# Kernel tuning notes

Measured on AMD Instinct MI355X. Metric: run time of the kernel, lower is better.

## Reference

```python
import jax, jax.numpy as jnp
import numpy as np

K, Q, DIM = 64, 128, 1024
TF_W, DE_W, FFT_W = 1.0, 0.8, 0.6  # opt.TF_weight / DE_weight / FFT_weight


def setup_inputs() -> dict:
    key = jax.random.key(0)
    ks = jax.random.split(key, 9)
    def feats(k):
        return jax.random.normal(k, (K, Q, DIM), dtype=jnp.float32)
    def protos(k):
        return jax.random.normal(k, (K, DIM), dtype=jnp.float32)
    def var(k):
        # positive variances, bounded away from zero
        return jax.random.uniform(k, (K,), dtype=jnp.float32) + 0.5
    return {
        "TFq_output": feats(ks[0]), "TFs_proto": protos(ks[1]), "TF_variance": var(ks[2]),
        "DEq_output": feats(ks[3]), "DEs_proto": protos(ks[4]), "DE_variance": var(ks[5]),
        "FFTq_output": feats(ks[6]), "FFTs_proto": protos(ks[7]), "FFT_variance": var(ks[8]),
    }


def _mah_dist(xq, proto, variance):
    # ||x - p||^2 / var via expansion: avoids materializing (num, protonum, dim)
    x2 = jnp.sum(xq * xq, axis=1, keepdims=True)            # (num, 1)
    p2 = jnp.sum(proto * proto, axis=1)[None, :]            # (1, protonum)
    xp = xq @ proto.T                                       # (num, protonum)
    return (x2 - 2.0 * xp + p2) / variance[None, :]


def _modality(xq, proto, variance, w):
    logits = -_mah_dist(xq, proto, variance)
    pred = w * jax.nn.softmax(logits, axis=1)
    mahloss = -(w * jax.nn.log_softmax(logits, axis=1))
    return pred, mahloss


def reference(TFq_output, TFs_proto, TF_variance,
              DEq_output, DEs_proto, DE_variance,
              FFTq_output, FFTs_proto, FFT_variance):
    k, q, _ = TFq_output.shape
    y = jnp.repeat(jnp.arange(k), q)                         # (k*q,)

    tf_pred, tf_loss = _modality(TFq_output.reshape(k * q, -1), TFs_proto, TF_variance, TF_W)
    de_pred, de_loss = _modality(DEq_output.reshape(k * q, -1), DEs_proto, DE_variance, DE_W)
    fft_pred, fft_loss = _modality(FFTq_output.reshape(k * q, -1), FFTs_proto, FFT_variance, FFT_W)

    fusion_loss = tf_loss + de_loss + fft_loss               # (k*q, k)
    loss = jnp.take_along_axis(fusion_loss, y[:, None], axis=1).squeeze(-1).mean()

    pred_mah = tf_pred + de_pred + fft_pred
    pred = jnp.argmax(pred_mah, axis=1)
    acc = (pred == y).astype(jnp.float32).mean()
    return (loss, acc)
```

## Files before the change

kernel.cpp:

```cpp
#include <hip/hip_runtime.h>


typedef _Float16 half8 __attribute__((ext_vector_type(8)));
typedef float    floatx4 __attribute__((ext_vector_type(4)));

#define NCLS   64
#define QPC    128
#define DIM    1024
#define NROWS  (NCLS * QPC)
#define NRT    (NROWS / 16)
#define CHUNK  256
#define NCHUNK (DIM / CHUNK)
#define NKC    (CHUNK / 32)
#define UW     264

#define OFF_W    0
#define W_BYTES  (3 * NCLS * DIM * 2)
#define OFF_P2   W_BYTES
#define OFF_PRED 397312
#define PRED_BYTES (3 * NROWS * NCLS * 4)
#define OFF_LOSS (OFF_PRED + PRED_BYTES)
#define OFF_CNT  (OFF_LOSS + 1536 * 4)
#define WS_NEED  (OFF_CNT + 64 * 4)

__device__ __forceinline__ void dma16(const float* g, float* l) {
    __builtin_amdgcn_global_load_lds(
        (const __attribute__((address_space(1))) void*)g,
        (__attribute__((address_space(3))) void*)l,
        16, 0, 0);
}

__global__ __launch_bounds__(64) void prep_protos(
    const float* __restrict__ Ptf, const float* __restrict__ Pde,
    const float* __restrict__ Pff, _Float16* __restrict__ W,
    float* __restrict__ p2)
{
    const int m    = blockIdx.x >> 5;
    const int kcg  = blockIdx.x & 31;
    const int lane = threadIdx.x;
    const int l15  = lane & 15;
    const int quad = lane >> 4;
    const float* __restrict__ P = (m == 0) ? Ptf : (m == 1) ? Pde : Pff;

    #pragma unroll
    for (int t = 0; t < 4; ++t) {
        const float* src = P + (size_t)(t * 16 + l15) * DIM + kcg * 32 + quad * 8;
        const float4 b0 = *reinterpret_cast<const float4*>(src);
        const float4 b1 = *reinterpret_cast<const float4*>(src + 4);
        half8 h;
        h[0] = (_Float16)b0.x; h[1] = (_Float16)b0.y;
        h[2] = (_Float16)b0.z; h[3] = (_Float16)b0.w;
        h[4] = (_Float16)b1.x; h[5] = (_Float16)b1.y;
        h[6] = (_Float16)b1.z; h[7] = (_Float16)b1.w;
        *reinterpret_cast<half8*>(W + ((size_t)(m * 32 + kcg) * 4 + t) * 512 + lane * 8) = h;

        float s = b0.x*b0.x + b0.y*b0.y + b0.z*b0.z + b0.w*b0.w
                + b1.x*b1.x + b1.y*b1.y + b1.z*b1.z + b1.w*b1.w;
        s += __shfl_xor(s, 16);
        s += __shfl_xor(s, 32);
        if (quad == 0) atomicAdd(&p2[m * 64 + t * 16 + l15], s);
    }
}

__global__ __launch_bounds__(128) void fusion_main(
    const float* __restrict__ Xtf, const float* __restrict__ Vtf,
    const float* __restrict__ Xde, const float* __restrict__ Vde,
    const float* __restrict__ Xff, const float* __restrict__ Vff,
    const _Float16* __restrict__ W, const float* __restrict__ p2g,
    float* __restrict__ predOut,
    float* __restrict__ lossPart)
{
    __shared__ float chunkBuf[16 * UW];
    __shared__ float mxW[2][16], sW[2][16];
    __shared__ float lossW[2];

    const int tid  = threadIdx.x;
    const int w    = tid >> 6;
    const int lane = tid & 63;
    const int l15  = lane & 15;
    const int quad = lane >> 4;
    const int m    = blockIdx.x >> 9;
    const int rt   = blockIdx.x & 511;
    const int rowBase = rt * 16;

    const float* __restrict__ X = (m == 0) ? Xtf : (m == 1) ? Xde : Xff;
    const float* __restrict__ V = (m == 0) ? Vtf : (m == 1) ? Vde : Vff;
    const float  wgt = (m == 0) ? 1.0f : (m == 1) ? 0.8f : 0.6f;

    floatx4 d[2];
    d[0] = (floatx4){0.f, 0.f, 0.f, 0.f};
    d[1] = (floatx4){0.f, 0.f, 0.f, 0.f};
    float x2p = 0.0f;

    #pragma unroll 1
    for (int c = 0; c < NCHUNK; ++c) {
        __syncthreads();
        const float* gbase = X + (size_t)rowBase * DIM + c * CHUNK + lane * 4;
        #pragma unroll
        for (int r8 = 0; r8 < 8; ++r8) {
            const int r = w * 8 + r8;
            dma16(gbase + (size_t)r * DIM, &chunkBuf[r * UW]);
        }
        __syncthreads();

        #pragma unroll
        for (int kc = 0; kc < NKC; ++kc) {
            const int off = l15 * UW + kc * 32 + quad * 8;
            const float4 a0 = *reinterpret_cast<const float4*>(&chunkBuf[off]);
            const float4 a1 = *reinterpret_cast<const float4*>(&chunkBuf[off + 4]);

            const int kcg = c * NKC + kc;
            half8 bf[2];
            #pragma unroll
            for (int t = 0; t < 2; ++t)
                bf[t] = *reinterpret_cast<const half8*>(
                    W + ((size_t)(m * 32 + kcg) * 4 + (w * 2 + t)) * 512 + lane * 8);

            x2p += a0.x*a0.x + a0.y*a0.y + a0.z*a0.z + a0.w*a0.w
                 + a1.x*a1.x + a1.y*a1.y + a1.z*a1.z + a1.w*a1.w;

            half8 af;
            af[0] = (_Float16)a0.x; af[1] = (_Float16)a0.y;
            af[2] = (_Float16)a0.z; af[3] = (_Float16)a0.w;
            af[4] = (_Float16)a1.x; af[5] = (_Float16)a1.y;
            af[6] = (_Float16)a1.z; af[7] = (_Float16)a1.w;

            d[0] = __builtin_amdgcn_mfma_f32_16x16x32_f16(af, bf[0], d[0], 0, 0, 0);
            d[1] = __builtin_amdgcn_mfma_f32_16x16x32_f16(af, bf[1], d[1], 0, 0, 0);
        }
    }

    x2p += __shfl_xor(x2p, 16);
    x2p += __shfl_xor(x2p, 32);
    float x2r[4];
    #pragma unroll
    for (int r = 0; r < 4; ++r) x2r[r] = __shfl(x2p, quad * 4 + r);

    float vc[2], p2c[2];
    #pragma unroll
    for (int t = 0; t < 2; ++t) {
        const int col = w * 32 + t * 16 + l15;
        vc[t]  = V[col];
        p2c[t] = p2g[m * 64 + col];
    }

    float lg[4][2];
    #pragma unroll
    for (int r = 0; r < 4; ++r)
        #pragma unroll
        for (int t = 0; t < 2; ++t)
            lg[r][t] = (2.0f * d[t][r] - x2r[r] - p2c[t]) / vc[t];

    #pragma unroll
    for (int r = 0; r < 4; ++r) {
        float mx = fmaxf(lg[r][0], lg[r][1]);
        #pragma unroll
        for (int dl = 1; dl <= 8; dl <<= 1) mx = fmaxf(mx, __shfl_xor(mx, dl));
        if (l15 == 0) mxW[w][quad * 4 + r] = mx;
    }
    __syncthreads();
    float gmx[4];
    #pragma unroll
    for (int r = 0; r < 4; ++r) {
        const int row = quad * 4 + r;
        gmx[r] = fmaxf(mxW[0][row], mxW[1][row]);
        float s = expf(lg[r][0] - gmx[r]) + expf(lg[r][1] - gmx[r]);
        #pragma unroll
        for (int dl = 1; dl <= 8; dl <<= 1) s += __shfl_xor(s, dl);
        if (l15 == 0) sW[w][row] = s;
    }
    __syncthreads();

    const int y = rowBase >> 7;
    float lossAcc = 0.0f;
    #pragma unroll
    for (int r = 0; r < 4; ++r) {
        const int row = quad * 4 + r;
        const float lse = gmx[r] + logf(sW[0][row] + sW[1][row]);
        if (w == (y >> 5) && l15 == (y & 15))
            lossAcc += wgt * (lse - lg[r][(y >> 4) & 1]);
        const int R = rowBase + row;
        #pragma unroll
        for (int t = 0; t < 2; ++t)
            predOut[((size_t)m * NROWS + R) * 64 + w * 32 + t * 16 + l15] =
                wgt * expf(lg[r][t] - lse);
    }

    #pragma unroll
    for (int dl = 1; dl <= 32; dl <<= 1) lossAcc += __shfl_xor(lossAcc, dl);
    if (lane == 0) lossW[w] = lossAcc;
    __syncthreads();
    if (tid == 0) lossPart[blockIdx.x] = lossW[0] + lossW[1];
}

__global__ __launch_bounds__(256) void finalize1(
    const float* __restrict__ pred, float* __restrict__ cntPart)
{
    const int tid  = threadIdx.x;
    const int w    = tid >> 6;
    const int lane = tid & 63;
    float cnt = 0.0f;
    #pragma unroll 1
    for (int i = 0; i < 32; ++i) {
        const int R = blockIdx.x * 128 + w * 32 + i;
        float p = pred[(size_t)R * 64 + lane]
                + pred[((size_t)NROWS + R) * 64 + lane]
                + pred[((size_t)2 * NROWS + R) * 64 + lane];
        float bv = p; int bc = lane;
        #pragma unroll
        for (int dl = 1; dl <= 32; dl <<= 1) {
            const float ov = __shfl_xor(bv, dl);
            const int   oc = __shfl_xor(bc, dl);
            if (ov > bv || (ov == bv && oc < bc)) { bv = ov; bc = oc; }
        }
        if (lane == 0 && bc == (R >> 7)) cnt += 1.0f;
    }
    #pragma unroll
    for (int dl = 1; dl <= 32; dl <<= 1) cnt += __shfl_xor(cnt, dl);
    __shared__ float sc[4];
    if (lane == 0) sc[w] = cnt;
    __syncthreads();
    if (tid == 0) cntPart[blockIdx.x] = sc[0] + sc[1] + sc[2] + sc[3];
}

__global__ __launch_bounds__(256) void finalize2(
    const float* __restrict__ lossPart, const float* __restrict__ cntPart,
    float* __restrict__ out)
{
    const int tid  = threadIdx.x;
    const int lane = tid & 63;
    const int w    = tid >> 6;
    float l = 0.0f, c = 0.0f;
    for (int i = tid; i < 1536; i += 256) l += lossPart[i];
    if (tid < 64) c = cntPart[tid];
    #pragma unroll
    for (int dl = 1; dl <= 32; dl <<= 1) {
        l += __shfl_xor(l, dl);
        c += __shfl_xor(c, dl);
    }
    __shared__ float sl[4], sc[4];
    if (lane == 0) { sl[w] = l; sc[w] = c; }
    __syncthreads();
    if (tid == 0) {
        out[0] = (sl[0] + sl[1] + sl[2] + sl[3]) * (1.0f / NROWS);
        out[1] = (sc[0] + sc[1] + sc[2] + sc[3]) * (1.0f / NROWS);
    }
}

#define NWAVES 12
#define KSPLIT 4
#define KSLICE (DIM / KSPLIT)
#define NITER  (KSLICE / 32)
#define DSTRIDE 17
#define PSTRIDE 65

__global__ __launch_bounds__(NWAVES * 64) void fusion_loss_fallback(
    const float* __restrict__ Xtf, const float* __restrict__ Ptf, const float* __restrict__ Vtf,
    const float* __restrict__ Xde, const float* __restrict__ Pde, const float* __restrict__ Vde,
    const float* __restrict__ Xff, const float* __restrict__ Pff, const float* __restrict__ Vff,
    float* __restrict__ out)
{
    __shared__ float dpart[NWAVES][64 * DSTRIDE];
    __shared__ float x2part[NWAVES][16];
    __shared__ float p2part[NWAVES][64];
    __shared__ float predL[16 * PSTRIDE];
    __shared__ float lossL;

    const int tid  = threadIdx.x;
    const int wave = tid >> 6;
    const int lane = tid & 63;
    const int l15  = lane & 15;
    const int quad = lane >> 4;
    const int m    = wave >> 2;
    const int kq   = wave & 3;
    const int rowBase = blockIdx.x * 16;

    for (int i = tid; i < 16 * PSTRIDE; i += NWAVES * 64) predL[i] = 0.0f;
    if (tid == 0) lossL = 0.0f;

    const float* __restrict__ X = (m == 0) ? Xtf : (m == 1) ? Xde : Xff;
    const float* __restrict__ P = (m == 0) ? Ptf : (m == 1) ? Pde : Pff;
    const float* __restrict__ V = (m == 0) ? Vtf : (m == 1) ? Vde : Vff;
    const float  w = (m == 0) ? 1.0f : (m == 1) ? 0.8f : 0.6f;

    floatx4 d[4];
    #pragma unroll
    for (int t = 0; t < 4; ++t) d[t] = (floatx4){0.f, 0.f, 0.f, 0.f};
    float x2p    = 0.0f;
    float p2p[4] = {0.f, 0.f, 0.f, 0.f};

    const float* xrow = X + (size_t)(rowBase + l15) * DIM + kq * KSLICE + quad * 8;
    const float* prow[4];
    #pragma unroll
    for (int t = 0; t < 4; ++t)
        prow[t] = P + (size_t)(t * 16 + l15) * DIM + kq * KSLICE + quad * 8;

    #pragma unroll 2
    for (int kc = 0; kc < NITER; ++kc) {
        const int ko = kc * 32;
        const float4 a0 = *reinterpret_cast<const float4*>(xrow + ko);
        const float4 a1 = *reinterpret_cast<const float4*>(xrow + ko + 4);
        float4 b0[4], b1[4];
        #pragma unroll
        for (int t = 0; t < 4; ++t) {
            b0[t] = *reinterpret_cast<const float4*>(prow[t] + ko);
            b1[t] = *reinterpret_cast<const float4*>(prow[t] + ko + 4);
        }
        x2p += a0.x*a0.x + a0.y*a0.y + a0.z*a0.z + a0.w*a0.w
             + a1.x*a1.x + a1.y*a1.y + a1.z*a1.z + a1.w*a1.w;
        half8 af;
        af[0] = (_Float16)a0.x; af[1] = (_Float16)a0.y;
        af[2] = (_Float16)a0.z; af[3] = (_Float16)a0.w;
        af[4] = (_Float16)a1.x; af[5] = (_Float16)a1.y;
        af[6] = (_Float16)a1.z; af[7] = (_Float16)a1.w;
        #pragma unroll
        for (int t = 0; t < 4; ++t) {
            p2p[t] += b0[t].x*b0[t].x + b0[t].y*b0[t].y + b0[t].z*b0[t].z + b0[t].w*b0[t].w
                    + b1[t].x*b1[t].x + b1[t].y*b1[t].y + b1[t].z*b1[t].z + b1[t].w*b1[t].w;
            half8 bf;
            bf[0] = (_Float16)b0[t].x; bf[1] = (_Float16)b0[t].y;
            bf[2] = (_Float16)b0[t].z; bf[3] = (_Float16)b0[t].w;
            bf[4] = (_Float16)b1[t].x; bf[5] = (_Float16)b1[t].y;
            bf[6] = (_Float16)b1[t].z; bf[7] = (_Float16)b1[t].w;
            d[t] = __builtin_amdgcn_mfma_f32_16x16x32_f16(af, bf, d[t], 0, 0, 0);
        }
    }

    x2p += __shfl_xor(x2p, 16);
    x2p += __shfl_xor(x2p, 32);
    #pragma unroll
    for (int t = 0; t < 4; ++t) {
        p2p[t] += __shfl_xor(p2p[t], 16);
        p2p[t] += __shfl_xor(p2p[t], 32);
    }
    {
        float* dp = &dpart[wave][lane * DSTRIDE];
        #pragma unroll
        for (int t = 0; t < 4; ++t)
            *reinterpret_cast<float4*>(dp + t * 4) =
                make_float4(d[t][0], d[t][1], d[t][2], d[t][3]);
        if (quad == 0) {
            x2part[wave][l15] = x2p;
            #pragma unroll
            for (int t = 0; t < 4; ++t) p2part[wave][t * 16 + l15] = p2p[t];
        }
    }
    __syncthreads();

    const int y = rowBase >> 7;

    if (kq == 0) {
        floatx4 dsum[4];
        #pragma unroll
        for (int t = 0; t < 4; ++t) dsum[t] = (floatx4){0.f, 0.f, 0.f, 0.f};
        float x2r[4] = {0.f, 0.f, 0.f, 0.f};
        float p2c[4] = {0.f, 0.f, 0.f, 0.f};
        #pragma unroll
        for (int k2 = 0; k2 < KSPLIT; ++k2) {
            const int wv = m * 4 + k2;
            const float* src = &dpart[wv][lane * DSTRIDE];
            #pragma unroll
            for (int t = 0; t < 4; ++t) {
                const float4 v = *reinterpret_cast<const float4*>(src + t * 4);
                dsum[t][0] += v.x; dsum[t][1] += v.y; dsum[t][2] += v.z; dsum[t][3] += v.w;
            }
            #pragma unroll
            for (int r = 0; r < 4; ++r) x2r[r] += x2part[wv][quad * 4 + r];
            #pragma unroll
            for (int t = 0; t < 4; ++t) p2c[t] += p2part[wv][t * 16 + l15];
        }
        float vc[4];
        #pragma unroll
        for (int t = 0; t < 4; ++t) vc[t] = V[t * 16 + l15];

        float lossAcc = 0.0f;
        #pragma unroll
        for (int r = 0; r < 4; ++r) {
            float lg[4];
            #pragma unroll
            for (int t = 0; t < 4; ++t)
                lg[t] = (2.0f * dsum[t][r] - x2r[r] - p2c[t]) / vc[t];
            float mx = fmaxf(fmaxf(lg[0], lg[1]), fmaxf(lg[2], lg[3]));
            #pragma unroll
            for (int dl = 1; dl <= 8; dl <<= 1) mx = fmaxf(mx, __shfl_xor(mx, dl));
            float s = expf(lg[0] - mx) + expf(lg[1] - mx)
                    + expf(lg[2] - mx) + expf(lg[3] - mx);
            #pragma unroll
            for (int dl = 1; dl <= 8; dl <<= 1) s += __shfl_xor(s, dl);
            const float lse = mx + logf(s);
            const int row = quad * 4 + r;
            #pragma unroll
            for (int t = 0; t < 4; ++t) {
                const int col = t * 16 + l15;
                if (col == y) lossAcc += w * (lse - lg[t]);
                atomicAdd(&predL[row * PSTRIDE + col], w * expf(lg[t] - lse));
            }
        }
        #pragma unroll
        for (int dl = 1; dl <= 32; dl <<= 1) lossAcc += __shfl_xor(lossAcc, dl);
        if (lane == 0) atomicAdd(&lossL, lossAcc);
    }
    __syncthreads();

    if (wave == 0) {
        float cnt = 0.0f;
        #pragma unroll 1
        for (int r = 0; r < 16; ++r) {
            float bv = predL[r * PSTRIDE + lane];
            int   bc = lane;
            #pragma unroll
            for (int dl = 1; dl <= 32; dl <<= 1) {
                const float ov = __shfl_xor(bv, dl);
                const int   oc = __shfl_xor(bc, dl);
                if (ov > bv || (ov == bv && oc < bc)) { bv = ov; bc = oc; }
            }
            if (lane == 0 && bc == y) cnt += 1.0f;
        }
        if (lane == 0) {
            atomicAdd(&out[0], lossL * (1.0f / NROWS));
            atomicAdd(&out[1], cnt * (1.0f / NROWS));
        }
    }
}

extern "C" void kernel_launch(void* const* d_in, const int* in_sizes, int n_in,
                              void* d_out, int out_size, void* d_ws, size_t ws_size,
                              hipStream_t stream) {
    const float* Xtf = (const float*)d_in[0];
    const float* Ptf = (const float*)d_in[1];
    const float* Vtf = (const float*)d_in[2];
    const float* Xde = (const float*)d_in[3];
    const float* Pde = (const float*)d_in[4];
    const float* Vde = (const float*)d_in[5];
    const float* Xff = (const float*)d_in[6];
    const float* Pff = (const float*)d_in[7];
    const float* Vff = (const float*)d_in[8];
    float* out = (float*)d_out;

    if (ws_size >= (size_t)WS_NEED) {
        char* ws = (char*)d_ws;
        _Float16* W    = (_Float16*)(ws + OFF_W);
        float*    p2   = (float*)(ws + OFF_P2);
        float*    pred = (float*)(ws + OFF_PRED);
        float*    lossP= (float*)(ws + OFF_LOSS);
        float*    cntP = (float*)(ws + OFF_CNT);

        hipMemsetAsync(p2, 0, 3 * NCLS * sizeof(float), stream);
        prep_protos<<<dim3(96), dim3(64), 0, stream>>>(Ptf, Pde, Pff, W, p2);
        fusion_main<<<dim3(3 * NRT), dim3(128), 0, stream>>>(
            Xtf, Vtf, Xde, Vde, Xff, Vff, W, p2, pred, lossP);
        finalize1<<<dim3(NROWS / 128), dim3(256), 0, stream>>>(pred, cntP);
        finalize2<<<dim3(1), dim3(256), 0, stream>>>(lossP, cntP, out);
    } else {
        hipMemsetAsync(out, 0, 2 * sizeof(float), stream);
        fusion_loss_fallback<<<dim3(NROWS / 16), dim3(NWAVES * 64), 0, stream>>>(
            Xtf, Ptf, Vtf, Xde, Pde, Vde, Xff, Pff, Vff, out);
    }
}
```

Measured before the change: 175.5 us.

## Split GEMM over K into two blocks and move softmax/loss into finalize

```diff
diff --git a/kernel.cpp b/kernel.cpp
--- a/kernel.cpp
+++ b/kernel.cpp
@@ -9,19 +9,18 @@
 #define DIM    1024
 #define NROWS  (NCLS * QPC)
 #define NRT    (NROWS / 16)
-#define CHUNK  256
-#define NCHUNK (DIM / CHUNK)
-#define NKC    (CHUNK / 32)
-#define UW     264
-
-#define OFF_W    0
-#define W_BYTES  (3 * NCLS * DIM * 2)
-#define OFF_P2   W_BYTES
-#define OFF_PRED 397312
-#define PRED_BYTES (3 * NROWS * NCLS * 4)
-#define OFF_LOSS (OFF_PRED + PRED_BYTES)
-#define OFF_CNT  (OFF_LOSS + 1536 * 4)
-#define WS_NEED  (OFF_CNT + 64 * 4)
+#define UW     260
+
+#define OFF_W     0
+#define W_BYTES   (3 * NCLS * DIM * 2)
+#define OFF_P2    W_BYTES
+#define OFF_PD    397312
+#define PD_BYTES  (3 * NRT * 2 * 16 * 64 * 4)
+#define OFF_PX2   (OFF_PD + PD_BYTES)
+#define PX2_BYTES (3 * NRT * 2 * 16 * 4)
+#define OFF_LP    (OFF_PX2 + PX2_BYTES)
+#define OFF_CP    (OFF_LP + NRT * 4)
+#define WS_NEED   (OFF_CP + NRT * 4)
 
 __device__ __forceinline__ void dma16(const float* g, float* l) {
     __builtin_amdgcn_global_load_lds(
@@ -62,59 +61,46 @@
     }
 }
 
-__global__ __launch_bounds__(128) void fusion_main(
-    const float* __restrict__ Xtf, const float* __restrict__ Vtf,
-    const float* __restrict__ Xde, const float* __restrict__ Vde,
-    const float* __restrict__ Xff, const float* __restrict__ Vff,
-    const _Float16* __restrict__ W, const float* __restrict__ p2g,
-    float* __restrict__ predOut,
-    float* __restrict__ lossPart)
+__global__ __launch_bounds__(256) void fusion_main(
+    const float* __restrict__ Xtf, const float* __restrict__ Xde,
+    const float* __restrict__ Xff, const _Float16* __restrict__ W,
+    float* __restrict__ pd, float* __restrict__ px2)
 {
     __shared__ float chunkBuf[16 * UW];
-    __shared__ float mxW[2][16], sW[2][16];
-    __shared__ float lossW[2];
 
     const int tid  = threadIdx.x;
     const int w    = tid >> 6;
     const int lane = tid & 63;
     const int l15  = lane & 15;
     const int quad = lane >> 4;
-    const int m    = blockIdx.x >> 9;
-    const int rt   = blockIdx.x & 511;
+    const int b    = blockIdx.x;
+    const int m    = b >> 10;
+    const int rt   = (b & 1023) >> 1;
+    const int ks   = b & 1;
     const int rowBase = rt * 16;
 
     const float* __restrict__ X = (m == 0) ? Xtf : (m == 1) ? Xde : Xff;
-    const float* __restrict__ V = (m == 0) ? Vtf : (m == 1) ? Vde : Vff;
-    const float  wgt = (m == 0) ? 1.0f : (m == 1) ? 0.8f : 0.6f;
-
-    floatx4 d[2];
-    d[0] = (floatx4){0.f, 0.f, 0.f, 0.f};
-    d[1] = (floatx4){0.f, 0.f, 0.f, 0.f};
+
+    floatx4 d = (floatx4){0.f, 0.f, 0.f, 0.f};
     float x2p = 0.0f;
 
     #pragma unroll 1
-    for (int c = 0; c < NCHUNK; ++c) {
+    for (int c = 0; c < 2; ++c) {
+        if (c) __syncthreads();
+        const float* gb = X + (size_t)(rowBase + w * 4) * DIM + ks * 512 + c * 256 + lane * 4;
+        #pragma unroll
+        for (int r4 = 0; r4 < 4; ++r4)
+            dma16(gb + (size_t)r4 * DIM, &chunkBuf[(w * 4 + r4) * UW]);
         __syncthreads();
-        const float* gbase = X + (size_t)rowBase * DIM + c * CHUNK + lane * 4;
-        #pragma unroll
-        for (int r8 = 0; r8 < 8; ++r8) {
-            const int r = w * 8 + r8;
-            dma16(gbase + (size_t)r * DIM, &chunkBuf[r * UW]);
-        }
-        __syncthreads();
-
-        #pragma unroll
-        for (int kc = 0; kc < NKC; ++kc) {
+
+        const int kbase = m * 32 + ks * 16 + c * 8;
+        #pragma unroll
+        for (int kc = 0; kc < 8; ++kc) {
             const int off = l15 * UW + kc * 32 + quad * 8;
             const float4 a0 = *reinterpret_cast<const float4*>(&chunkBuf[off]);
             const float4 a1 = *reinterpret_cast<const float4*>(&chunkBuf[off + 4]);
-
-            const int kcg = c * NKC + kc;
-            half8 bf[2];
-            #pragma unroll
-            for (int t = 0; t < 2; ++t)
-                bf[t] = *reinterpret_cast<const half8*>(
-                    W + ((size_t)(m * 32 + kcg) * 4 + (w * 2 + t)) * 512 + lane * 8);
+            const half8 bf = *reinterpret_cast<const half8*>(
+                W + ((size_t)(kbase + kc) * 4 + w) * 512 + lane * 8);
 
             x2p += a0.x*a0.x + a0.y*a0.y + a0.z*a0.z + a0.w*a0.w
                  + a1.x*a1.x + a1.y*a1.y + a1.z*a1.z + a1.w*a1.w;
@@ -125,102 +111,84 @@
             af[4] = (_Float16)a1.x; af[5] = (_Float16)a1.y;
             af[6] = (_Float16)a1.z; af[7] = (_Float16)a1.w;
 
-            d[0] = __builtin_amdgcn_mfma_f32_16x16x32_f16(af, bf[0], d[0], 0, 0, 0);
-            d[1] = __builtin_amdgcn_mfma_f32_16x16x32_f16(af, bf[1], d[1], 0, 0, 0);
+            d = __builtin_amdgcn_mfma_f32_16x16x32_f16(af, bf, d, 0, 0, 0);
         }
     }
 
     x2p += __shfl_xor(x2p, 16);
     x2p += __shfl_xor(x2p, 32);
-    float x2r[4];
-    #pragma unroll
-    for (int r = 0; r < 4; ++r) x2r[r] = __shfl(x2p, quad * 4 + r);
-
-    float vc[2], p2c[2];
-    #pragma unroll
-    for (int t = 0; t < 2; ++t) {
-        const int col = w * 32 + t * 16 + l15;
-        vc[t]  = V[col];
-        p2c[t] = p2g[m * 64 + col];
-    }
-
-    float lg[4][2];
+
+    const size_t tb = (size_t)((m * NRT + rt) * 2 + ks);
+    if (w == 0 && quad == 0) px2[tb * 16 + l15] = x2p;
+
+    float* o = pd + tb * 1024;
     #pragma unroll
     for (int r = 0; r < 4; ++r)
-        #pragma unroll
-        for (int t = 0; t < 2; ++t)
-            lg[r][t] = (2.0f * d[t][r] - x2r[r] - p2c[t]) / vc[t];
-
-    #pragma unroll
-    for (int r = 0; r < 4; ++r) {
-        float mx = fmaxf(lg[r][0], lg[r][1]);
-        #pragma unroll
-        for (int dl = 1; dl <= 8; dl <<= 1) mx = fmaxf(mx, __shfl_xor(mx, dl));
-        if (l15 == 0) mxW[w][quad * 4 + r] = mx;
-    }
-    __syncthreads();
-    float gmx[4];
-    #pragma unroll
-    for (int r = 0; r < 4; ++r) {
-        const int row = quad * 4 + r;
-        gmx[r] = fmaxf(mxW[0][row], mxW[1][row]);
-        float s = expf(lg[r][0] - gmx[r]) + expf(lg[r][1] - gmx[r]);
-        #pragma unroll
-        for (int dl = 1; dl <= 8; dl <<= 1) s += __shfl_xor(s, dl);
-        if (l15 == 0) sW[w][row] = s;
-    }
-    __syncthreads();
-
-    const int y = rowBase >> 7;
-    float lossAcc = 0.0f;
-    #pragma unroll
-    for (int r = 0; r < 4; ++r) {
-        const int row = quad * 4 + r;
-        const float lse = gmx[r] + logf(sW[0][row] + sW[1][row]);
-        if (w == (y >> 5) && l15 == (y & 15))
-            lossAcc += wgt * (lse - lg[r][(y >> 4) & 1]);
-        const int R = rowBase + row;
-        #pragma unroll
-        for (int t = 0; t < 2; ++t)
-            predOut[((size_t)m * NROWS + R) * 64 + w * 32 + t * 16 + l15] =
-                wgt * expf(lg[r][t] - lse);
-    }
-
-    #pragma unroll
-    for (int dl = 1; dl <= 32; dl <<= 1) lossAcc += __shfl_xor(lossAcc, dl);
-    if (lane == 0) lossW[w] = lossAcc;
-    __syncthreads();
-    if (tid == 0) lossPart[blockIdx.x] = lossW[0] + lossW[1];
+        o[(quad * 4 + r) * 64 + w * 16 + l15] = d[r];
 }
 
 __global__ __launch_bounds__(256) void finalize1(
-    const float* __restrict__ pred, float* __restrict__ cntPart)
+    const float* __restrict__ pd, const float* __restrict__ px2,
+    const float* __restrict__ p2g,
+    const float* __restrict__ Vtf, const float* __restrict__ Vde,
+    const float* __restrict__ Vff,
+    float* __restrict__ lossPart, float* __restrict__ cntPart)
 {
+    const int rt   = blockIdx.x;
     const int tid  = threadIdx.x;
-    const int w    = tid >> 6;
+    const int v    = tid >> 6;
     const int lane = tid & 63;
-    float cnt = 0.0f;
-    #pragma unroll 1
-    for (int i = 0; i < 32; ++i) {
-        const int R = blockIdx.x * 128 + w * 32 + i;
-        float p = pred[(size_t)R * 64 + lane]
-                + pred[((size_t)NROWS + R) * 64 + lane]
-                + pred[((size_t)2 * NROWS + R) * 64 + lane];
-        float bv = p; int bc = lane;
+
+    float loss = 0.0f, cnt = 0.0f;
+    #pragma unroll
+    for (int r4 = 0; r4 < 4; ++r4) {
+        const int row = v * 4 + r4;
+        const int R   = rt * 16 + row;
+        const int y   = R >> 7;
+        float pf = 0.0f;
+        #pragma unroll
+        for (int m = 0; m < 3; ++m) {
+            const size_t t0 = (size_t)((m * NRT + rt) * 2);
+            const float dsum = pd[t0 * 1024 + row * 64 + lane]
+                             + pd[(t0 + 1) * 1024 + row * 64 + lane];
+            const float x2 = px2[t0 * 16 + row] + px2[(t0 + 1) * 16 + row];
+            const float* __restrict__ V = (m == 0) ? Vtf : (m == 1) ? Vde : Vff;
+            const float wgt = (m == 0) ? 1.0f : (m == 1) ? 0.8f : 0.6f;
+
+            const float lg = (2.0f * dsum - x2 - p2g[m * 64 + lane]) / V[lane];
+            float mx = lg;
+            #pragma unroll
+            for (int dl = 1; dl <= 32; dl <<= 1) mx = fmaxf(mx, __shfl_xor(mx, dl));
+            float s = expf(lg - mx);
+            #pragma unroll
+            for (int dl = 1; dl <= 32; dl <<= 1) s += __shfl_xor(s, dl);
+            const float lse = mx + logf(s);
+
+            if (lane == y) loss += wgt * (lse - lg);
+            pf += wgt * expf(lg - lse);
+        }
+        float bv = pf; int bc = lane;
         #pragma unroll
         for (int dl = 1; dl <= 32; dl <<= 1) {
             const float ov = __shfl_xor(bv, dl);
             const int   oc = __shfl_xor(bc, dl);
             if (ov > bv || (ov == bv && oc < bc)) { bv = ov; bc = oc; }
         }
-        if (lane == 0 && bc == (R >> 7)) cnt += 1.0f;
-    }
-    #pragma unroll
-    for (int dl = 1; dl <= 32; dl <<= 1) cnt += __shfl_xor(cnt, dl);
-    __shared__ float sc[4];
-    if (lane == 0) sc[w] = cnt;
+        if (lane == 0 && bc == y) cnt += 1.0f;
+    }
+
+    #pragma unroll
+    for (int dl = 1; dl <= 32; dl <<= 1) {
+        loss += __shfl_xor(loss, dl);
+        cnt  += __shfl_xor(cnt, dl);
+    }
+    __shared__ float sl[4], sc[4];
+    if (lane == 0) { sl[v] = loss; sc[v] = cnt; }
     __syncthreads();
-    if (tid == 0) cntPart[blockIdx.x] = sc[0] + sc[1] + sc[2] + sc[3];
+    if (tid == 0) {
+        lossPart[rt] = sl[0] + sl[1] + sl[2] + sl[3];
+        cntPart[rt]  = sc[0] + sc[1] + sc[2] + sc[3];
+    }
 }
 
 __global__ __launch_bounds__(256) void finalize2(
@@ -229,17 +197,16 @@
 {
     const int tid  = threadIdx.x;
     const int lane = tid & 63;
-    const int w    = tid >> 6;
+    const int v    = tid >> 6;
     float l = 0.0f, c = 0.0f;
-    for (int i = tid; i < 1536; i += 256) l += lossPart[i];
-    if (tid < 64) c = cntPart[tid];
+    for (int i = tid; i < NRT; i += 256) { l += lossPart[i]; c += cntPart[i]; }
     #pragma unroll
     for (int dl = 1; dl <= 32; dl <<= 1) {
         l += __shfl_xor(l, dl);
         c += __shfl_xor(c, dl);
     }
     __shared__ float sl[4], sc[4];
-    if (lane == 0) { sl[w] = l; sc[w] = c; }
+    if (lane == 0) { sl[v] = l; sc[v] = c; }
     __syncthreads();
     if (tid == 0) {
         out[0] = (sl[0] + sl[1] + sl[2] + sl[3]) * (1.0f / NROWS);
@@ -361,8 +328,8 @@
             const float* src = &dpart[wv][lane * DSTRIDE];
             #pragma unroll
             for (int t = 0; t < 4; ++t) {
-                const float4 v = *reinterpret_cast<const float4*>(src + t * 4);
-                dsum[t][0] += v.x; dsum[t][1] += v.y; dsum[t][2] += v.z; dsum[t][3] += v.w;
+                const float4 vv = *reinterpret_cast<const float4*>(src + t * 4);
+                dsum[t][0] += vv.x; dsum[t][1] += vv.y; dsum[t][2] += vv.z; dsum[t][3] += vv.w;
             }
             #pragma unroll
             for (int r = 0; r < 4; ++r) x2r[r] += x2part[wv][quad * 4 + r];
@@ -439,17 +406,19 @@
 
     if (ws_size >= (size_t)WS_NEED) {
         char* ws = (char*)d_ws;
-        _Float16* W    = (_Float16*)(ws + OFF_W);
-        float*    p2   = (float*)(ws + OFF_P2);
-        float*    pred = (float*)(ws + OFF_PRED);
-        float*    lossP= (float*)(ws + OFF_LOSS);
-        float*    cntP = (float*)(ws + OFF_CNT);
+        _Float16* W     = (_Float16*)(ws + OFF_W);
+        float*    p2    = (float*)(ws + OFF_P2);
+        float*    pd    = (float*)(ws + OFF_PD);
+        float*    px2   = (float*)(ws + OFF_PX2);
+        float*    lossP = (float*)(ws + OFF_LP);
+        float*    cntP  = (float*)(ws + OFF_CP);
 
         hipMemsetAsync(p2, 0, 3 * NCLS * sizeof(float), stream);
         prep_protos<<<dim3(96), dim3(64), 0, stream>>>(Ptf, Pde, Pff, W, p2);
-        fusion_main<<<dim3(3 * NRT), dim3(128), 0, stream>>>(
-            Xtf, Vtf, Xde, Vde, Xff, Vff, W, p2, pred, lossP);
-        finalize1<<<dim3(NROWS / 128), dim3(256), 0, stream>>>(pred, cntP);
+        fusion_main<<<dim3(3 * NRT * 2), dim3(256), 0, stream>>>(
+            Xtf, Xde, Xff, W, pd, px2);
+        finalize1<<<dim3(NRT), dim3(256), 0, stream>>>(
+            pd, px2, p2, Vtf, Vde, Vff, lossP, cntP);
         finalize2<<<dim3(1), dim3(256), 0, stream>>>(lossP, cntP, out);
     } else {
         hipMemsetAsync(out, 0, 2 * sizeof(float), stream);
```

Measured after the change: 157.1 us. 1.12x faster.
